# Kernel optimization log

Measured on AMD Instinct MI355X. Metric: run time of the kernel, lower is better.

Reference implementation:

```python
import jax, jax.numpy as jnp
import numpy as np

B, T, D, H = 2, 2048, 1024, 16
DK = D // H


def setup_inputs() -> dict:
    key = jax.random.key(0)
    ks = jax.random.split(key, 12)
    s = 0.02
    return {
        "query": jax.random.normal(ks[0], (B, T, D), jnp.float32),
        "key": jax.random.normal(ks[1], (B, T, D), jnp.float32),
        "value": jax.random.normal(ks[2], (B, T, D), jnp.float32),
        "mask": jax.random.randint(ks[3], (B, T), 0, 2) != 0,  # True = keep
        "Wq": jax.random.normal(ks[4], (D, D), jnp.float32) * s,
        "bq": jnp.zeros((D,), jnp.float32),
        "Wk": jax.random.normal(ks[5], (D, D), jnp.float32) * s,
        "bk": jnp.zeros((D,), jnp.float32),
        "Wv": jax.random.normal(ks[6], (D, D), jnp.float32) * s,
        "bv": jnp.zeros((D,), jnp.float32),
        "Wo": jax.random.normal(ks[7], (D, D), jnp.float32) * s,
        "bo": jnp.zeros((D,), jnp.float32),
    }


def _split_heads(x):
    # [B, S, D] -> [B, H, S, DK]
    b, s, _ = x.shape
    return x.reshape(b, s, H, DK).transpose(0, 2, 1, 3)


def reference(query, key, value, mask, Wq, bq, Wk, bk, Wv, bv, Wo, bo):
    # torch Linear: y = x @ W.T + b
    q = _split_heads(query @ Wq.T + bq)   # [B,H,T,DK]
    k = _split_heads(key @ Wk.T + bk)     # [B,H,S,DK]
    v = _split_heads(value @ Wv.T + bv)   # [B,H,S,DK]
    scale = 1.0 / np.sqrt(DK).astype(np.float32)
    scores = jnp.einsum('bhtd,bhsd->bhts', q, k) * scale  # [B,H,T,S]
    # key-padding mask [B,S] -> broadcast [B,1,1,S], True = keep
    scores = jnp.where(mask[:, None, None, :], scores, -jnp.inf)
    attn = jax.nn.softmax(scores, axis=-1)
    out = jnp.einsum('bhts,bhsd->bhtd', attn, v)           # [B,H,T,DK]
    out = out.transpose(0, 2, 1, 3).reshape(query.shape[0], -1, D)
    return out @ Wo.T + bo
```

## Files before the change

### kernel.cpp

```cpp
#include <hip/hip_runtime.h>
#include <stdint.h>

#define B_SZ 2
#define T_SEQ 2048
#define DMODEL 1024
#define NHEAD 16
#define DKH 64
#define M_ROWS (B_SZ * T_SEQ)

#define LDT 72

#define INP_E  4194304u
#define W_E    1048576u

typedef __bf16 bf16x8 __attribute__((ext_vector_type(8)));
typedef float  f32x4  __attribute__((ext_vector_type(4)));

__device__ __forceinline__ unsigned short f2bf(float f) {
    unsigned u = __builtin_bit_cast(unsigned, f);
    u += 0x7fffu + ((u >> 16) & 1u);
    return (unsigned short)(u >> 16);
}
__device__ __forceinline__ uint4 cvt8(const float* p) {
    float4 f0 = *(const float4*)p, f1 = *(const float4*)(p + 4);
    uint4 r;
    r.x = (unsigned)f2bf(f0.x) | ((unsigned)f2bf(f0.y) << 16);
    r.y = (unsigned)f2bf(f0.z) | ((unsigned)f2bf(f0.w) << 16);
    r.z = (unsigned)f2bf(f1.x) | ((unsigned)f2bf(f1.y) << 16);
    r.w = (unsigned)f2bf(f1.z) | ((unsigned)f2bf(f1.w) << 16);
    return r;
}

__device__ __forceinline__ void async16(const unsigned short* g, unsigned short* l) {
    __builtin_amdgcn_global_load_lds(
        (const __attribute__((address_space(1))) void*)g,
        (__attribute__((address_space(3))) void*)l, 16, 0, 0);
}

__global__ __launch_bounds__(256) void cvt_all(
    const float* __restrict__ q, const float* __restrict__ k, const float* __restrict__ v,
    const float* __restrict__ wq, const float* __restrict__ wk,
    const float* __restrict__ wv, const float* __restrict__ wo,
    unsigned short* __restrict__ wsb)
{
    int blk = blockIdx.x;
    const float* src; unsigned short* dst; int lb;
    if      (blk < 2048) { src = q;  dst = wsb;                       lb = blk; }
    else if (blk < 4096) { src = k;  dst = wsb + INP_E;               lb = blk - 2048; }
    else if (blk < 6144) { src = v;  dst = wsb + 2 * INP_E;           lb = blk - 4096; }
    else if (blk < 6656) { src = wq; dst = wsb + 3 * INP_E;           lb = blk - 6144; }
    else if (blk < 7168) { src = wk; dst = wsb + 3 * INP_E + W_E;     lb = blk - 6656; }
    else if (blk < 7680) { src = wv; dst = wsb + 3 * INP_E + 2 * W_E; lb = blk - 7168; }
    else                 { src = wo; dst = wsb + 3 * INP_E + 3 * W_E; lb = blk - 7680; }
    size_t i = ((size_t)lb * 256 + threadIdx.x) * 8;
    *(uint4*)&dst[i] = cvt8(src + i);
}

template<int C_MODE, int MT>
__device__ __forceinline__ void gemm_core(
    const unsigned short* __restrict__ A, const unsigned short* __restrict__ W,
    const float* __restrict__ bias, void* __restrict__ C,
    int N, int K, int bx, int by,
    unsigned short* sA, unsigned short* sB)
{
    const int tid  = threadIdx.x;
    const int wave = tid >> 6, lane = tid & 63;
    const int quad = lane >> 4, l15 = lane & 15;
    const int TM = MT * 32;
    const int m0 = by * TM, n0 = bx * 128;
    const int wm = (wave & 1) * (MT * 16), wn = (wave >> 1) * 64;

    f32x4 acc[MT][4] = {};

    for (int k0 = 0; k0 < K; k0 += 64) {
        __syncthreads();
        #pragma unroll
        for (int i = 0; i < MT; i++) {
            int c   = tid + 256 * i;
            int row = c >> 3;
            int gk  = ((c & 7) ^ (row & 7)) * 8;
            int sb  = (wave * 64 + 256 * i) * 8;
            async16(&A[(size_t)(m0 + row) * K + k0 + gk], sA + sb);
        }
        #pragma unroll
        for (int i = 0; i < 4; i++) {
            int c   = tid + 256 * i;
            int row = c >> 3;
            int gk  = ((c & 7) ^ (row & 7)) * 8;
            int sb  = (wave * 64 + 256 * i) * 8;
            async16(&W[(size_t)(n0 + row) * K + k0 + gk], sB + sb);
        }
        __syncthreads();
        const int sw = l15 & 7;
        #pragma unroll
        for (int ks = 0; ks < 2; ks++) {
            bf16x8 af[MT], bfv[4];
            #pragma unroll
            for (int mt = 0; mt < MT; mt++)
                af[mt] = *(const bf16x8*)&sA[(wm + mt * 16 + l15) * 64 +
                                             (((ks * 4 + quad) ^ sw) * 8)];
            #pragma unroll
            for (int nt = 0; nt < 4; nt++)
                bfv[nt] = *(const bf16x8*)&sB[(wn + nt * 16 + l15) * 64 +
                                              (((ks * 4 + quad) ^ sw) * 8)];
            #pragma unroll
            for (int mt = 0; mt < MT; mt++)
                #pragma unroll
                for (int nt = 0; nt < 4; nt++)
                    acc[mt][nt] = __builtin_amdgcn_mfma_f32_16x16x32_bf16(
                        af[mt], bfv[nt], acc[mt][nt], 0, 0, 0);
        }
    }

    if (C_MODE == 2) {
        #pragma unroll
        for (int mt = 0; mt < MT; mt++) {
            #pragma unroll
            for (int r = 0; r < 4; r++) {
                int m = m0 + wm + mt * 16 + quad * 4 + r;
                float bm = bias[m];
                #pragma unroll
                for (int nt = 0; nt < 4; nt++) {
                    int n = n0 + wn + nt * 16 + l15;
                    int bb = n >> 11, t = n & 2047;
                    ((unsigned short*)C)[((size_t)bb * 1024 + m) * 2048 + t] =
                        f2bf(acc[mt][nt][r] + bm);
                }
            }
        }
    } else {
        #pragma unroll
        for (int nt = 0; nt < 4; nt++) {
            int n = n0 + wn + nt * 16 + l15;
            float bv = bias[n];
            #pragma unroll
            for (int mt = 0; mt < MT; mt++) {
                #pragma unroll
                for (int r = 0; r < 4; r++) {
                    int m = m0 + wm + mt * 16 + quad * 4 + r;
                    float val = acc[mt][nt][r] + bv;
                    if (C_MODE == 1) ((float*)C)[(size_t)m * N + n] = val;
                    else ((unsigned short*)C)[(size_t)m * N + n] = f2bf(val);
                }
            }
        }
    }
}

__global__ __launch_bounds__(256) void gemm_qkv(
    const unsigned short* __restrict__ Qb, const unsigned short* __restrict__ Kb,
    const unsigned short* __restrict__ Vb,
    const unsigned short* __restrict__ Wqb, const unsigned short* __restrict__ Wkb,
    const unsigned short* __restrict__ Wvb,
    const float* __restrict__ bq, const float* __restrict__ bk, const float* __restrict__ bv,
    unsigned short* __restrict__ Qp, unsigned short* __restrict__ Kp,
    unsigned short* __restrict__ Vt)
{
    __shared__ __align__(16) unsigned short sA[128 * 64];
    __shared__ __align__(16) unsigned short sB[128 * 64];
    const int z = blockIdx.z, id = blockIdx.x;
    if (z < 2) {
        gemm_core<0, 4>(z ? Kb : Qb, z ? Wkb : Wqb, z ? bk : bq, z ? Kp : Qp,
                        DMODEL, DMODEL, id & 7, id >> 3, sA, sB);
    } else {
        gemm_core<2, 4>(Wvb, Vb, bv, Vt, M_ROWS, DMODEL, id & 31, id >> 5, sA, sB);
    }
}

__global__ __launch_bounds__(256) void gemm_o(
    const unsigned short* __restrict__ AO, const unsigned short* __restrict__ Wob,
    const float* __restrict__ bo, float* __restrict__ out)
{
    __shared__ __align__(16) unsigned short sA[64 * 64];
    __shared__ __align__(16) unsigned short sB[128 * 64];
    const int id = blockIdx.x;
    gemm_core<1, 2>(AO, Wob, bo, out, DMODEL, DMODEL, id & 7, id >> 3, sA, sB);
}

__global__ __launch_bounds__(256) void attn_kernel(
    const unsigned short* __restrict__ Qp,
    const unsigned short* __restrict__ Kp,
    const unsigned short* __restrict__ Vt,
    const int* __restrict__ maskp,
    unsigned short* __restrict__ Op)
{
    __shared__ __align__(16) unsigned short sK[64 * 64];
    __shared__ __align__(16) unsigned short sV[64 * 64];
    __shared__ __align__(16) unsigned short sP[4 * 16 * LDT];
    __shared__ float smask[64];

    const int tid  = threadIdx.x;
    const int wave = tid >> 6, lane = tid & 63;
    const int quad = lane >> 4, l15 = lane & 15;
    const int qblk = blockIdx.x, h = blockIdx.y, b = blockIdx.z;

    const float SCL2 = 0.125f * 1.44269504089f;
    const float MNEG = -30000.f;

    const int qrow = qblk * 64 + wave * 16 + l15;
    const unsigned short* qptr = Qp + (size_t)(b * T_SEQ + qrow) * DMODEL + h * DKH + quad * 8;
    const bf16x8 aq0 = *(const bf16x8*)qptr;
    const bf16x8 aq1 = *(const bf16x8*)(qptr + 32);

    const unsigned short* Kb_ = Kp + (size_t)b * T_SEQ * DMODEL + h * DKH;
    const unsigned short* VtB = Vt + ((size_t)b * DMODEL + h * DKH) * T_SEQ;

    f32x4 O[4] = {};
    float l_r[4] = {0.f, 0.f, 0.f, 0.f};
    unsigned short* sPw = sP + wave * 16 * LDT;

    for (int s0 = 0; s0 < T_SEQ; s0 += 64) {
        __syncthreads();
        #pragma unroll
        for (int i = 0; i < 2; i++) {
            int c   = tid + 256 * i;
            int row = c >> 3;
            int gk  = ((c & 7) ^ (row & 7)) * 8;
            int sb  = (wave * 64 + 256 * i) * 8;
            async16(&Kb_[(size_t)(s0 + row) * DMODEL + gk], sK + sb);
            async16(&VtB[(size_t)row * T_SEQ + s0 + gk], sV + sb);
        }
        if (tid < 64)
            smask[tid] = maskp[b * T_SEQ + s0 + tid] ? 0.f : MNEG;
        __syncthreads();

        const int sw = l15 & 7;
        f32x4 S[4];
        #pragma unroll
        for (int nt = 0; nt < 4; nt++) {
            const unsigned short* kr = &sK[(nt * 16 + l15) * 64];
            f32x4 z = {};
            z = __builtin_amdgcn_mfma_f32_16x16x32_bf16(
                aq0, *(const bf16x8*)&kr[(quad ^ sw) * 8], z, 0, 0, 0);
            z = __builtin_amdgcn_mfma_f32_16x16x32_bf16(
                aq1, *(const bf16x8*)&kr[((quad + 4) ^ sw) * 8], z, 0, 0, 0);
            S[nt] = z;
        }

        #pragma unroll
        for (int nt = 0; nt < 4; nt++) {
            float madd = smask[nt * 16 + l15];
            #pragma unroll
            for (int r = 0; r < 4; r++) {
                float p = __builtin_amdgcn_exp2f(fmaf(S[nt][r], SCL2, madd));
                l_r[r] += p;
                unsigned u = __builtin_bit_cast(unsigned, p) + 0x8000u;
                sPw[(quad * 4 + r) * LDT + nt * 16 + l15] = (unsigned short)(u >> 16);
            }
        }
        __syncthreads();

        const bf16x8 ap0 = *(const bf16x8*)&sPw[l15 * LDT + quad * 8];
        const bf16x8 ap1 = *(const bf16x8*)&sPw[l15 * LDT + 32 + quad * 8];
        #pragma unroll
        for (int nt = 0; nt < 4; nt++) {
            const unsigned short* vr = &sV[(nt * 16 + l15) * 64];
            O[nt] = __builtin_amdgcn_mfma_f32_16x16x32_bf16(
                ap0, *(const bf16x8*)&vr[(quad ^ sw) * 8], O[nt], 0, 0, 0);
            O[nt] = __builtin_amdgcn_mfma_f32_16x16x32_bf16(
                ap1, *(const bf16x8*)&vr[((quad + 4) ^ sw) * 8], O[nt], 0, 0, 0);
        }
    }

    #pragma unroll
    for (int r = 0; r < 4; r++) {
        float l = l_r[r];
        l += __shfl_xor(l, 1);
        l += __shfl_xor(l, 2);
        l += __shfl_xor(l, 4);
        l += __shfl_xor(l, 8);
        l_r[r] = 1.0f / fmaxf(l, 1e-30f);
    }
    #pragma unroll
    for (int nt = 0; nt < 4; nt++) {
        #pragma unroll
        for (int r = 0; r < 4; r++) {
            int q = qblk * 64 + wave * 16 + quad * 4 + r;
            Op[(size_t)(b * T_SEQ + q) * DMODEL + h * DKH + nt * 16 + l15] =
                f2bf(O[nt][r] * l_r[r]);
        }
    }
}

template<int A_BF16, int W_BF16, int C_MODE>
__global__ __launch_bounds__(256) void gemm_bt_cvt(
    const void* __restrict__ A_, const void* __restrict__ W_,
    const float* __restrict__ bias, void* __restrict__ C_,
    int M, int N, int K)
{
    __shared__ __align__(16) unsigned short sA[128 * LDT];
    __shared__ __align__(16) unsigned short sB[128 * LDT];
    const int tid  = threadIdx.x;
    const int wave = tid >> 6, lane = tid & 63;
    const int quad = lane >> 4, l15 = lane & 15;
    const int m0 = blockIdx.y * 128, n0 = blockIdx.x * 128;
    const int wm = (wave & 1) * 64, wn = (wave >> 1) * 64;
    f32x4 acc[4][4] = {};
    for (int k0 = 0; k0 < K; k0 += 64) {
        __syncthreads();
        #pragma unroll
        for (int i = 0; i < 4; i++) {
            int c = tid + 256 * i;
            int row = c >> 3, koff = (c & 7) * 8;
            if (A_BF16)
                *(uint4*)&sA[row * LDT + koff] =
                    *(const uint4*)&((const unsigned short*)A_)[(size_t)(m0 + row) * K + k0 + koff];
            else
                *(uint4*)&sA[row * LDT + koff] =
                    cvt8((const float*)A_ + (size_t)(m0 + row) * K + k0 + koff);
            if (W_BF16)
                *(uint4*)&sB[row * LDT + koff] =
                    *(const uint4*)&((const unsigned short*)W_)[(size_t)(n0 + row) * K + k0 + koff];
            else
                *(uint4*)&sB[row * LDT + koff] =
                    cvt8((const float*)W_ + (size_t)(n0 + row) * K + k0 + koff);
        }
        __syncthreads();
        #pragma unroll
        for (int ks = 0; ks < 2; ks++) {
            bf16x8 af[4], bfr[4];
            #pragma unroll
            for (int mt = 0; mt < 4; mt++)
                af[mt] = *(const bf16x8*)&sA[(wm + mt * 16 + l15) * LDT + ks * 32 + quad * 8];
            #pragma unroll
            for (int nt = 0; nt < 4; nt++)
                bfr[nt] = *(const bf16x8*)&sB[(wn + nt * 16 + l15) * LDT + ks * 32 + quad * 8];
            #pragma unroll
            for (int mt = 0; mt < 4; mt++)
                #pragma unroll
                for (int nt = 0; nt < 4; nt++)
                    acc[mt][nt] = __builtin_amdgcn_mfma_f32_16x16x32_bf16(
                        af[mt], bfr[nt], acc[mt][nt], 0, 0, 0);
        }
    }
    if (C_MODE == 2) {
        #pragma unroll
        for (int mt = 0; mt < 4; mt++)
            #pragma unroll
            for (int r = 0; r < 4; r++) {
                int m = m0 + wm + mt * 16 + quad * 4 + r;
                float bm = bias[m];
                #pragma unroll
                for (int nt = 0; nt < 4; nt++) {
                    int n = n0 + wn + nt * 16 + l15;
                    int bb = n >> 11, t = n & 2047;
                    ((unsigned short*)C_)[((size_t)bb * 1024 + m) * 2048 + t] =
                        f2bf(acc[mt][nt][r] + bm);
                }
            }
    } else {
        #pragma unroll
        for (int nt = 0; nt < 4; nt++) {
            int n = n0 + wn + nt * 16 + l15;
            float bv = bias[n];
            #pragma unroll
            for (int mt = 0; mt < 4; mt++)
                #pragma unroll
                for (int r = 0; r < 4; r++) {
                    int m = m0 + wm + mt * 16 + quad * 4 + r;
                    float val = acc[mt][nt][r] + bv;
                    if (C_MODE == 1) ((float*)C_)[(size_t)m * N + n] = val;
                    else ((unsigned short*)C_)[(size_t)m * N + n] = f2bf(val);
                }
        }
    }
}

extern "C" void kernel_launch(void* const* d_in, const int* in_sizes, int n_in,
                              void* d_out, int out_size, void* d_ws, size_t ws_size,
                              hipStream_t stream)
{
    const float* q  = (const float*)d_in[0];
    const float* k  = (const float*)d_in[1];
    const float* v  = (const float*)d_in[2];
    const int*   mk = (const int*)d_in[3];
    const float* Wq = (const float*)d_in[4];
    const float* bq = (const float*)d_in[5];
    const float* Wk = (const float*)d_in[6];
    const float* bk = (const float*)d_in[7];
    const float* Wv = (const float*)d_in[8];
    const float* bv = (const float*)d_in[9];
    const float* Wo = (const float*)d_in[10];
    const float* bo = (const float*)d_in[11];
    float* out = (float*)d_out;

    unsigned short* wsb = (unsigned short*)d_ws;
    const dim3 gA(T_SEQ / 64, NHEAD, B_SZ);

    if (ws_size >= (size_t)64 * 1024 * 1024) {
        unsigned short* Qb  = wsb;
        unsigned short* Kb  = wsb + INP_E;
        unsigned short* Vb  = wsb + 2 * INP_E;
        unsigned short* Wqb = wsb + 3 * INP_E;
        unsigned short* Wkb = wsb + 3 * INP_E + W_E;
        unsigned short* Wvb = wsb + 3 * INP_E + 2 * W_E;
        unsigned short* Wob = wsb + 3 * INP_E + 3 * W_E;
        unsigned short* Qp  = wsb + 4 * INP_E;
        unsigned short* Kp  = wsb + 5 * INP_E;
        unsigned short* Vt  = wsb + 6 * INP_E;
        unsigned short* AO  = wsb + 7 * INP_E;

        cvt_all<<<8192, 256, 0, stream>>>(q, k, v, Wq, Wk, Wv, Wo, wsb);
        gemm_qkv<<<dim3(256, 1, 3), 256, 0, stream>>>(
            Qb, Kb, Vb, Wqb, Wkb, Wvb, bq, bk, bv, Qp, Kp, Vt);
        attn_kernel<<<gA, 256, 0, stream>>>(Qp, Kp, Vt, mk, AO);
        gemm_o<<<dim3(512, 1, 1), 256, 0, stream>>>(AO, Wob, bo, out);
    } else {
        unsigned short* Qp = wsb;
        unsigned short* Kp = wsb + INP_E;
        unsigned short* Vt = wsb + 2 * INP_E;
        unsigned short* AO = wsb + 3 * INP_E;
        const dim3 gN(DMODEL / 128, M_ROWS / 128);
        const dim3 gV(M_ROWS / 128, DMODEL / 128);
        gemm_bt_cvt<0, 0, 0><<<gN, 256, 0, stream>>>(q, Wq, bq, Qp, M_ROWS, DMODEL, DMODEL);
        gemm_bt_cvt<0, 0, 0><<<gN, 256, 0, stream>>>(k, Wk, bk, Kp, M_ROWS, DMODEL, DMODEL);
        gemm_bt_cvt<0, 0, 2><<<gV, 256, 0, stream>>>(Wv, v, bv, Vt, DMODEL, M_ROWS, DMODEL);
        attn_kernel<<<gA, 256, 0, stream>>>(Qp, Kp, Vt, mk, AO);
        gemm_bt_cvt<1, 0, 1><<<gN, 256, 0, stream>>>(AO, Wo, bo, out, M_ROWS, DMODEL, DMODEL);
    }
}
```

Measured before the change: 242.1 us.

## Double-buffer K/V tiles in attention with 128-row query blocks and fewer barriers

The attention kernel now uses 512-thread blocks that each cover 128 query rows, and it double-buffers the K and V shared-memory tiles. The next 64-key tile is prefetched asynchronously while the current one is being computed, so each iteration needs one barrier instead of three. The whole key mask is preloaded into shared memory once per block, and the MFMA sections are raised to a higher wave priority. In exchange, shared-memory use and block size grow, and there are half as many blocks (512 over 256 CUs), which may reduce latency hiding and leave some CUs with uneven work.

Result: faster. 234.6 us (-3.1%).

```diff
diff --git a/kernel.cpp b/kernel.cpp
--- a/kernel.cpp
+++ b/kernel.cpp
@@ -177,17 +177,20 @@
     gemm_core<1, 2>(AO, Wob, bo, out, DMODEL, DMODEL, id & 7, id >> 3, sA, sB);
 }
 
-__global__ __launch_bounds__(256) void attn_kernel(
+#define QBLK 128
+#define KVB 64
+
+__global__ __launch_bounds__(512) void attn_kernel(
     const unsigned short* __restrict__ Qp,
     const unsigned short* __restrict__ Kp,
     const unsigned short* __restrict__ Vt,
     const int* __restrict__ maskp,
     unsigned short* __restrict__ Op)
 {
-    __shared__ __align__(16) unsigned short sK[64 * 64];
-    __shared__ __align__(16) unsigned short sV[64 * 64];
-    __shared__ __align__(16) unsigned short sP[4 * 16 * LDT];
-    __shared__ float smask[64];
+    __shared__ __align__(16) unsigned short sK[2][KVB * 64];
+    __shared__ __align__(16) unsigned short sV[2][KVB * 64];
+    __shared__ __align__(16) unsigned short sP[8 * 16 * LDT];
+    __shared__ float smf[T_SEQ];
 
     const int tid  = threadIdx.x;
     const int wave = tid >> 6, lane = tid & 63;
@@ -197,7 +200,7 @@
     const float SCL2 = 0.125f * 1.44269504089f;
     const float MNEG = -30000.f;
 
-    const int qrow = qblk * 64 + wave * 16 + l15;
+    const int qrow = qblk * QBLK + wave * 16 + l15;
     const unsigned short* qptr = Qp + (size_t)(b * T_SEQ + qrow) * DMODEL + h * DKH + quad * 8;
     const bf16x8 aq0 = *(const bf16x8*)qptr;
     const bf16x8 aq1 = *(const bf16x8*)(qptr + 32);
@@ -205,30 +208,38 @@
     const unsigned short* Kb_ = Kp + (size_t)b * T_SEQ * DMODEL + h * DKH;
     const unsigned short* VtB = Vt + ((size_t)b * DMODEL + h * DKH) * T_SEQ;
 
+    const int src_ = tid;
+    const int srow = src_ >> 3;
+    const int sgk  = ((src_ & 7) ^ (srow & 7)) * 8;
+    const int ssb  = wave * 512;
+
     f32x4 O[4] = {};
     float l_r[4] = {0.f, 0.f, 0.f, 0.f};
     unsigned short* sPw = sP + wave * 16 * LDT;
 
-    for (int s0 = 0; s0 < T_SEQ; s0 += 64) {
-        __syncthreads();
-        #pragma unroll
-        for (int i = 0; i < 2; i++) {
-            int c   = tid + 256 * i;
-            int row = c >> 3;
-            int gk  = ((c & 7) ^ (row & 7)) * 8;
-            int sb  = (wave * 64 + 256 * i) * 8;
-            async16(&Kb_[(size_t)(s0 + row) * DMODEL + gk], sK + sb);
-            async16(&VtB[(size_t)row * T_SEQ + s0 + gk], sV + sb);
-        }
-        if (tid < 64)
-            smask[tid] = maskp[b * T_SEQ + s0 + tid] ? 0.f : MNEG;
-        __syncthreads();
-
-        const int sw = l15 & 7;
+    async16(&Kb_[(size_t)srow * DMODEL + sgk], &sK[0][ssb]);
+    async16(&VtB[(size_t)srow * T_SEQ + sgk], &sV[0][ssb]);
+    #pragma unroll
+    for (int j = 0; j < 4; j++) {
+        int i = tid + 512 * j;
+        smf[i] = maskp[b * T_SEQ + i] ? 0.f : MNEG;
+    }
+    __syncthreads();
+
+    const int sw = l15 & 7;
+    for (int t = 0; t < T_SEQ / KVB; ++t) {
+        const int cur = t & 1;
+        const int s0 = t * KVB;
+        if (t + 1 < T_SEQ / KVB) {
+            async16(&Kb_[(size_t)(s0 + KVB + srow) * DMODEL + sgk], &sK[cur ^ 1][ssb]);
+            async16(&VtB[(size_t)srow * T_SEQ + s0 + KVB + sgk], &sV[cur ^ 1][ssb]);
+        }
+
         f32x4 S[4];
+        __builtin_amdgcn_s_setprio(1);
         #pragma unroll
         for (int nt = 0; nt < 4; nt++) {
-            const unsigned short* kr = &sK[(nt * 16 + l15) * 64];
+            const unsigned short* kr = &sK[cur][(nt * 16 + l15) * 64];
             f32x4 z = {};
             z = __builtin_amdgcn_mfma_f32_16x16x32_bf16(
                 aq0, *(const bf16x8*)&kr[(quad ^ sw) * 8], z, 0, 0, 0);
@@ -236,10 +247,11 @@
                 aq1, *(const bf16x8*)&kr[((quad + 4) ^ sw) * 8], z, 0, 0, 0);
             S[nt] = z;
         }
+        __builtin_amdgcn_s_setprio(0);
 
         #pragma unroll
         for (int nt = 0; nt < 4; nt++) {
-            float madd = smask[nt * 16 + l15];
+            float madd = smf[s0 + nt * 16 + l15];
             #pragma unroll
             for (int r = 0; r < 4; r++) {
                 float p = __builtin_amdgcn_exp2f(fmaf(S[nt][r], SCL2, madd));
@@ -248,18 +260,21 @@
                 sPw[(quad * 4 + r) * LDT + nt * 16 + l15] = (unsigned short)(u >> 16);
             }
         }
-        __syncthreads();
 
         const bf16x8 ap0 = *(const bf16x8*)&sPw[l15 * LDT + quad * 8];
         const bf16x8 ap1 = *(const bf16x8*)&sPw[l15 * LDT + 32 + quad * 8];
+        __builtin_amdgcn_s_setprio(1);
         #pragma unroll
         for (int nt = 0; nt < 4; nt++) {
-            const unsigned short* vr = &sV[(nt * 16 + l15) * 64];
+            const unsigned short* vr = &sV[cur][(nt * 16 + l15) * 64];
             O[nt] = __builtin_amdgcn_mfma_f32_16x16x32_bf16(
                 ap0, *(const bf16x8*)&vr[(quad ^ sw) * 8], O[nt], 0, 0, 0);
             O[nt] = __builtin_amdgcn_mfma_f32_16x16x32_bf16(
                 ap1, *(const bf16x8*)&vr[((quad + 4) ^ sw) * 8], O[nt], 0, 0, 0);
         }
+        __builtin_amdgcn_s_setprio(0);
+
+        __syncthreads();
     }
 
     #pragma unroll
@@ -275,7 +290,7 @@
     for (int nt = 0; nt < 4; nt++) {
         #pragma unroll
         for (int r = 0; r < 4; r++) {
-            int q = qblk * 64 + wave * 16 + quad * 4 + r;
+            int q = qblk * QBLK + wave * 16 + quad * 4 + r;
             Op[(size_t)(b * T_SEQ + q) * DMODEL + h * DKH + nt * 16 + l15] =
                 f2bf(O[nt][r] * l_r[r]);
         }
@@ -385,7 +400,7 @@
     float* out = (float*)d_out;
 
     unsigned short* wsb = (unsigned short*)d_ws;
-    const dim3 gA(T_SEQ / 64, NHEAD, B_SZ);
+    const dim3 gA(T_SEQ / QBLK, NHEAD, B_SZ);
 
     if (ws_size >= (size_t)64 * 1024 * 1024) {
         unsigned short* Qb  = wsb;
@@ -403,7 +418,7 @@
         cvt_all<<<8192, 256, 0, stream>>>(q, k, v, Wq, Wk, Wv, Wo, wsb);
         gemm_qkv<<<dim3(256, 1, 3), 256, 0, stream>>>(
             Qb, Kb, Vb, Wqb, Wkb, Wvb, bq, bk, bv, Qp, Kp, Vt);
-        attn_kernel<<<gA, 256, 0, stream>>>(Qp, Kp, Vt, mk, AO);
+        attn_kernel<<<gA, 512, 0, stream>>>(Qp, Kp, Vt, mk, AO);
         gemm_o<<<dim3(512, 1, 1), 256, 0, stream>>>(AO, Wob, bo, out);
     } else {
         unsigned short* Qp = wsb;
@@ -415,7 +430,7 @@
         gemm_bt_cvt<0, 0, 0><<<gN, 256, 0, stream>>>(q, Wq, bq, Qp, M_ROWS, DMODEL, DMODEL);
         gemm_bt_cvt<0, 0, 0><<<gN, 256, 0, stream>>>(k, Wk, bk, Kp, M_ROWS, DMODEL, DMODEL);
         gemm_bt_cvt<0, 0, 2><<<gV, 256, 0, stream>>>(Wv, v, bv, Vt, DMODEL, M_ROWS, DMODEL);
-        attn_kernel<<<gA, 256, 0, stream>>>(Qp, Kp, Vt, mk, AO);
+        attn_kernel<<<gA, 512, 0, stream>>>(Qp, Kp, Vt, mk, AO);
         gemm_bt_cvt<1, 0, 1><<<gN, 256, 0, stream>>>(AO, Wo, bo, out, M_ROWS, DMODEL, DMODEL);
     }
 }
```
